# Optimization experiments

Hardware: AMD Instinct MI355X
Metric: run time of the kernel (lower is better)

The kernel has to match this reference:

```python
import jax, jax.numpy as jnp
import numpy as np

HEADS = 4
DIM_HEAD = 64
MAP_SIZE = 16
SCALE = DIM_HEAD ** (-0.5)


def _split_heads(x):
    # torch rearrange 'b (dim_head heads) h w -> b heads (h w) dim_head'
    B, C, H, W = x.shape
    x = x.reshape(B, DIM_HEAD, HEADS, H * W)
    return jnp.transpose(x, (0, 2, 3, 1))  # [B, heads, N, dim_head]


def _merge_heads(x, H, W):
    # torch rearrange 'b heads (h w) dim_head -> b (dim_head heads) h w'
    B, h, N, d = x.shape
    return jnp.transpose(x, (0, 3, 1, 2)).reshape(B, d * h, H, W)


def setup_inputs() -> dict:
    key = jax.random.key(0)
    ks = jax.random.split(key, 6)
    feat = jax.random.normal(ks[0], (4, 256, 96, 96), jnp.float32)
    semantic_map = jax.random.normal(ks[1], (4, 256, 16, 16), jnp.float32)
    # 1x1 conv weights, shape [out_ch, in_ch]; scaled like fan-in init
    W_feat_qv = 0.05 * jax.random.normal(ks[2], (512, 256), jnp.float32)
    W_map_qv = 0.05 * jax.random.normal(ks[3], (512, 256), jnp.float32)
    W_feat_out = 0.05 * jax.random.normal(ks[4], (256, 256), jnp.float32)
    W_map_out = 0.05 * jax.random.normal(ks[5], (256, 256), jnp.float32)
    return {
        "feat": feat,
        "semantic_map": semantic_map,
        "W_feat_qv": W_feat_qv,
        "W_map_qv": W_map_qv,
        "W_feat_out": W_feat_out,
        "W_map_out": W_map_out,
    }


def reference(feat, semantic_map, W_feat_qv, W_map_qv, W_feat_out, W_map_out):
    B, C, H, W = feat.shape
    # 1x1 convs == per-pixel channel matmuls
    fqv = jnp.einsum("oc,bchw->bohw", W_feat_qv, feat)
    feat_q, feat_v = jnp.split(fqv, 2, axis=1)
    mqv = jnp.einsum("oc,bchw->bohw", W_map_qv, semantic_map)
    map_q, map_v = jnp.split(mqv, 2, axis=1)

    feat_q, feat_v = _split_heads(feat_q), _split_heads(feat_v)  # [B,h,N,d]
    map_q, map_v = _split_heads(map_q), _split_heads(map_v)      # [B,h,M,d]

    attn = jnp.einsum("bhid,bhjd->bhij", feat_q, map_q) * SCALE  # [B,h,N,M]
    feat_map_attn = jax.nn.softmax(attn, axis=-1)  # normalize over map tokens j
    map_feat_attn = jax.nn.softmax(attn, axis=-2)  # normalize over feat tokens i

    feat_o = jnp.einsum("bhij,bhjd->bhid", feat_map_attn, map_v)   # [B,h,N,d]
    map_o = jnp.einsum("bhji,bhjd->bhid", map_feat_attn, feat_v)   # [B,h,M,d]

    feat_o = _merge_heads(feat_o, H, W)
    map_o = _merge_heads(map_o, MAP_SIZE, MAP_SIZE)

    feat_out = jnp.einsum("oc,bchw->bohw", W_feat_out, feat_o)
    map_out = jnp.einsum("oc,bchw->bohw", W_map_out, map_o)
    return feat_out, map_out
```

## Files before the change

kernel.cpp:

```cpp
#include <hip/hip_runtime.h>
#include <stdint.h>

#define DI static __device__ __forceinline__

constexpr int NTOK = 9216;
constexpr float ATT_SCALE = 0.125f;

typedef short bf16x8 __attribute__((ext_vector_type(8)));
typedef float f32x4  __attribute__((ext_vector_type(4)));

DI f32x4 mfma16(bf16x8 a, bf16x8 b, f32x4 c) {
  return __builtin_amdgcn_mfma_f32_16x16x32_bf16(a, b, c, 0, 0, 0);
}

DI float lo2f(uint32_t u) { union { uint32_t i; float f; } v; v.i = u << 16; return v.f; }
DI float hi2f(uint32_t u) { union { uint32_t i; float f; } v; v.i = u & 0xffff0000u; return v.f; }
DI float b2f(uint16_t u) { union { uint32_t i; float f; } v; v.i = ((uint32_t)u) << 16; return v.f; }
DI uint16_t f2b(float f) {
  union { float f; uint32_t i; } v; v.f = f;
  uint32_t r = (v.i + 0x7fffu + ((v.i >> 16) & 1u)) >> 16;
  return (uint16_t)r;
}

template<int DT> DI float ld1(const void* p, size_t off) {
  if constexpr (DT) return b2f(((const uint16_t*)p)[off]);
  else              return ((const float*)p)[off];
}
template<int DT> DI void st1(void* p, size_t off, float v) {
  if constexpr (DT) ((uint16_t*)p)[off] = f2b(v);
  else              ((float*)p)[off] = v;
}
template<int DT> DI void load8(const void* p, size_t off, float* o) {
  if constexpr (DT) {
    const uint4 w = *(const uint4*)((const uint16_t*)p + off);
    o[0] = lo2f(w.x); o[1] = hi2f(w.x); o[2] = lo2f(w.y); o[3] = hi2f(w.y);
    o[4] = lo2f(w.z); o[5] = hi2f(w.z); o[6] = lo2f(w.w); o[7] = hi2f(w.w);
  } else {
    const float4 a = *(const float4*)((const float*)p + off);
    const float4 b = *(const float4*)((const float*)p + off + 4);
    o[0] = a.x; o[1] = a.y; o[2] = a.z; o[3] = a.w;
    o[4] = b.x; o[5] = b.y; o[6] = b.z; o[7] = b.w;
  }
}

__global__ void detect_dtype(const uint32_t* __restrict__ w, int* __restrict__ flag) {
  if (threadIdx.x == 0 && blockIdx.x == 0) {
    int cl = 0;
    for (int i = 0; i < 256; ++i) {
      const float b = b2f((uint16_t)(w[i] & 0xffffu));
      const float ab = fabsf(b);
      if (ab > 1e-4f && ab < 0.5f) cl++;
    }
    flag[0] = (cl >= 128) ? 1 : 0;
  }
}

template<int DT>
__global__ __launch_bounds__(256) void prep_w(
    const void* __restrict__ Wfqv, const void* __restrict__ Wfo,
    uint16_t* __restrict__ WqvP, uint16_t* __restrict__ WfoP,
    const int* __restrict__ flag)
{
  if (flag[0] != DT) return;
  const int r = blockIdx.x, c = threadIdx.x;
  if (r < 512) {
    const int sel = r >> 8, within = r & 255;
    const int h = within >> 6, d = within & 63;
    const int src = sel * 256 + d * 4 + h;
    const int q = (c >> 3) & 3, j = c & 7;
    const int kp = (c & ~31) | (q << 3) | ((j + 2 * q) & 7);
    WqvP[(size_t)r * 256 + c] = f2b(ld1<DT>(Wfqv, (size_t)src * 256 + kp));
  } else {
    const int ro = r - 512;
    WfoP[(size_t)ro * 256 + c] =
        f2b(ld1<DT>(Wfo, (size_t)ro * 256 + (c & 63) * 4 + (c >> 6)));
  }
}

constexpr int PB = 264;

template<int DT>
__global__ __launch_bounds__(256) void gemm0_mfma(
    const uint16_t* __restrict__ WqvP, const void* __restrict__ X,
    uint16_t* __restrict__ FQ, uint16_t* __restrict__ FV,
    const int* __restrict__ flag)
{
  if (flag[0] != DT) return;
  __shared__ __align__(16) uint16_t Bsh[32 * PB];
  const int tid = threadIdx.x;
  const int w = tid >> 6, lane = tid & 63;
  const int l = lane & 15, quad = lane >> 4;
  const int n0 = blockIdx.x * 256;
  const int hh = blockIdx.y;
  const int bb = blockIdx.z;
  const size_t bh = (size_t)bb * 4 + hh;

  f32x4 acc[8][4];
  #pragma unroll
  for (int a = 0; a < 8; ++a)
    #pragma unroll
    for (int b = 0; b < 4; ++b) { acc[a][b].x = 0.f; acc[a][b].y = 0.f; acc[a][b].z = 0.f; acc[a][b].w = 0.f; }

  const int cst = tid >> 3;
  const int nst = (tid & 7) * 32;

  for (int ks = 0; ks < 8; ++ks) {
    {
      const size_t gbase = ((size_t)bb * 256 + ks * 32 + cst) * NTOK + n0 + nst;
      #pragma unroll
      for (int q = 0; q < 4; ++q) {
        if constexpr (DT) {
          *(uint4*)(Bsh + cst * PB + nst + q * 8) =
              *(const uint4*)((const uint16_t*)X + gbase + q * 8);
        } else {
          float xv[8];
          load8<0>(X, gbase + q * 8, xv);
          uint16_t pk[8];
          #pragma unroll
          for (int j = 0; j < 8; ++j) pk[j] = f2b(xv[j]);
          *(uint4*)(Bsh + cst * PB + nst + q * 8) = *(const uint4*)pk;
        }
      }
    }
    __syncthreads();
    bf16x8 af[8];
    #pragma unroll
    for (int mt = 0; mt < 8; ++mt) {
      const int arow = (mt >> 2) * 256 + hh * 64 + (mt & 3) * 16 + l;
      af[mt] = *(const bf16x8*)(WqvP + (size_t)arow * 256 + ks * 32 + quad * 8);
    }
    #pragma unroll
    for (int nt = 0; nt < 4; ++nt) {
      const int nl = w * 64 + nt * 16 + l;
      union { uint16_t h[8]; bf16x8 v; } bu;
      #pragma unroll
      for (int j = 0; j < 8; ++j)
        bu.h[j] = Bsh[(quad * 8 + ((j + 2 * quad) & 7)) * PB + nl];
      #pragma unroll
      for (int mt = 0; mt < 8; ++mt)
        acc[mt][nt] = mfma16(af[mt], bu.v, acc[mt][nt]);
    }
    __syncthreads();
  }
  #pragma unroll
  for (int mt = 0; mt < 8; ++mt)
    #pragma unroll
    for (int nt = 0; nt < 4; ++nt) {
      const int n = n0 + w * 64 + nt * 16 + l;
      if (mt < 4) {
        union { uint16_t h[4]; uint2 u; } pk;
        #pragma unroll
        for (int r = 0; r < 4; ++r) pk.h[r] = f2b(acc[mt][nt][r]);
        *(uint2*)(FQ + (bh * NTOK + n) * 64 + mt * 16 + quad * 4) = pk.u;
      } else {
        #pragma unroll
        for (int r = 0; r < 4; ++r)
          FV[(bh * 64 + (mt - 4) * 16 + quad * 4 + r) * NTOK + n] =
              f2b(acc[mt][nt][r]);
      }
    }
}

template<int DT>
__global__ __launch_bounds__(256) void gemm1_mfma(
    const uint16_t* __restrict__ WfoP, const uint16_t* __restrict__ FO,
    void* __restrict__ out, const int* __restrict__ flag)
{
  if (flag[0] != DT) return;
  const int tid = threadIdx.x;
  const int w = tid >> 6, lane = tid & 63;
  const int l = lane & 15, quad = lane >> 4;
  const int n0 = blockIdx.x * 256;
  const int o0 = blockIdx.y * 64;
  const int bb = blockIdx.z;

  f32x4 acc[4][4];
  #pragma unroll
  for (int a = 0; a < 4; ++a)
    #pragma unroll
    for (int b = 0; b < 4; ++b) { acc[a][b].x = 0.f; acc[a][b].y = 0.f; acc[a][b].z = 0.f; acc[a][b].w = 0.f; }

  for (int ks = 0; ks < 8; ++ks) {
    const int h2 = ks >> 1;
    const int doff = (ks & 1) * 32 + quad * 8;
    bf16x8 af[4];
    #pragma unroll
    for (int mt = 0; mt < 4; ++mt)
      af[mt] = *(const bf16x8*)(WfoP + (size_t)(o0 + mt * 16 + l) * 256 + ks * 32 + quad * 8);
    #pragma unroll
    for (int nt = 0; nt < 4; ++nt) {
      const int n = n0 + w * 64 + nt * 16 + l;
      const bf16x8 bv = *(const bf16x8*)(FO + ((size_t)(bb * 4 + h2) * NTOK + n) * 64 + doff);
      #pragma unroll
      for (int mt = 0; mt < 4; ++mt)
        acc[mt][nt] = mfma16(af[mt], bv, acc[mt][nt]);
    }
  }
  #pragma unroll
  for (int mt = 0; mt < 4; ++mt)
    #pragma unroll
    for (int nt = 0; nt < 4; ++nt) {
      const int n = n0 + w * 64 + nt * 16 + l;
      #pragma unroll
      for (int r = 0; r < 4; ++r)
        st1<DT>(out, ((size_t)bb * 256 + o0 + mt * 16 + quad * 4 + r) * NTOK + n,
                acc[mt][nt][r]);
    }
}

template<int DT>
__global__ __launch_bounds__(256) void map_qv(
    const void* __restrict__ Wqv, const void* __restrict__ smap,
    uint16_t* __restrict__ MQ, uint16_t* __restrict__ MVT,
    const int* __restrict__ flag)
{
  if (flag[0] != DT) return;
  const int o = blockIdx.x, bb = blockIdx.y, m = threadIdx.x;
  float acc = 0.f;
  #pragma unroll 8
  for (int c = 0; c < 256; ++c)
    acc += ld1<DT>(Wqv, (size_t)o * 256 + c) *
           ld1<DT>(smap, (size_t)bb * 65536 + (size_t)c * 256 + m);
  const int oc = o & 255;
  const int h = oc & 3, d = oc >> 2;
  if (o < 256) MQ[(((size_t)bb * 4 + h) * 256 + m) * 64 + d] = f2b(acc);
  else         MVT[(((size_t)bb * 4 + h) * 64 + d) * 256 + m] = f2b(acc);
}

constexpr int PJ = 264;
constexpr int PI = 48;
constexpr int NGRP = 32;

__global__ __launch_bounds__(256, 3) void attn_mfma(
    const uint16_t* __restrict__ FQ, const uint16_t* __restrict__ FV,
    const uint16_t* __restrict__ MQ, const uint16_t* __restrict__ MVT,
    uint16_t* __restrict__ FO, uint16_t* __restrict__ P)
{
  __shared__ __align__(16) uint16_t Esh[32 * PJ];
  __shared__ __align__(16) uint16_t ETsh[256 * PI];
  __shared__ float RS[4][32];
  const int tid = threadIdx.x;
  const int w = tid >> 6;
  const int lane = tid & 63;
  const int l = lane & 15, quad = lane >> 4;
  const int blk = blockIdx.x, bh = blockIdx.y;
  const uint16_t* FQh  = FQ  + (size_t)bh * NTOK * 64;
  const uint16_t* FVh  = FV  + (size_t)bh * 64 * NTOK;
  const uint16_t* MQh  = MQ  + (size_t)bh * 256 * 64;
  const uint16_t* MVTh = MVT + (size_t)bh * 64 * 256;
  uint16_t* FOh = FO + (size_t)bh * NTOK * 64;

  f32x4 numacc[4][4];
  #pragma unroll
  for (int a = 0; a < 4; ++a)
    #pragma unroll
    for (int b = 0; b < 4; ++b) { numacc[a][b].x = 0.f; numacc[a][b].y = 0.f; numacc[a][b].z = 0.f; numacc[a][b].w = 0.f; }
  float csum[4] = {0.f, 0.f, 0.f, 0.f};

  for (int t = 0; t < 9; ++t) {
    const int i0 = (blk * 9 + t) * 32;

    bf16x8 qa[2][2];
    #pragma unroll
    for (int mt = 0; mt < 2; ++mt)
      #pragma unroll
      for (int kb = 0; kb < 2; ++kb)
        qa[mt][kb] = *(const bf16x8*)(FQh + (size_t)(i0 + mt * 16 + l) * 64 + kb * 32 + quad * 8);
    float rsum[2][4] = {{0.f,0.f,0.f,0.f},{0.f,0.f,0.f,0.f}};
    #pragma unroll
    for (int jt = 0; jt < 4; ++jt) {
      const int j0 = w * 64 + jt * 16;
      const bf16x8 kb0 = *(const bf16x8*)(MQh + (size_t)(j0 + l) * 64 + quad * 8);
      const bf16x8 kb1 = *(const bf16x8*)(MQh + (size_t)(j0 + l) * 64 + 32 + quad * 8);
      #pragma unroll
      for (int mt = 0; mt < 2; ++mt) {
        f32x4 acc = {0.f, 0.f, 0.f, 0.f};
        acc = mfma16(qa[mt][0], kb0, acc);
        acc = mfma16(qa[mt][1], kb1, acc);
        union { uint16_t h[4]; uint2 u; } pk;
        #pragma unroll
        for (int r = 0; r < 4; ++r) {
          const float e = __expf(acc[r] * ATT_SCALE);
          rsum[mt][r] += e;
          csum[jt] += e;
          pk.h[r] = f2b(e);
          Esh[(mt * 16 + quad * 4 + r) * PJ + j0 + l] = pk.h[r];
        }
        *(uint2*)(ETsh + (size_t)(j0 + l) * PI + mt * 16 + quad * 4) = pk.u;
      }
    }
    #pragma unroll
    for (int mt = 0; mt < 2; ++mt)
      #pragma unroll
      for (int r = 0; r < 4; ++r) {
        float v = rsum[mt][r];
        v += __shfl_xor(v, 1); v += __shfl_xor(v, 2);
        v += __shfl_xor(v, 4); v += __shfl_xor(v, 8);
        if (l == 0) RS[w][mt * 16 + quad * 4 + r] = v;
      }
    __syncthreads();

    {
      float rinv[2];
      #pragma unroll
      for (int nt = 0; nt < 2; ++nt) {
        const int i_ = nt * 16 + l;
        rinv[nt] = 1.f / (RS[0][i_] + RS[1][i_] + RS[2][i_] + RS[3][i_]);
      }
      f32x4 oacc[2];
      oacc[0].x=0.f;oacc[0].y=0.f;oacc[0].z=0.f;oacc[0].w=0.f;
      oacc[1]=oacc[0];
      #pragma unroll
      for (int ks = 0; ks < 8; ++ks) {
        const bf16x8 av = *(const bf16x8*)(MVTh + (size_t)(w * 16 + l) * 256 + ks * 32 + quad * 8);
        #pragma unroll
        for (int nt = 0; nt < 2; ++nt) {
          const bf16x8 bv = *(const bf16x8*)(Esh + (size_t)(nt * 16 + l) * PJ + ks * 32 + quad * 8);
          oacc[nt] = mfma16(av, bv, oacc[nt]);
        }
      }
      #pragma unroll
      for (int nt = 0; nt < 2; ++nt) {
        union { uint16_t h[4]; uint2 u; } pk;
        #pragma unroll
        for (int r = 0; r < 4; ++r) pk.h[r] = f2b(oacc[nt][r] * rinv[nt]);
        *(uint2*)(FOh + (size_t)(i0 + nt * 16 + l) * 64 + w * 16 + quad * 4) = pk.u;
      }
    }

    #pragma unroll
    for (int mt = 0; mt < 4; ++mt) {
      const bf16x8 av = *(const bf16x8*)(FVh + (size_t)(mt * 16 + l) * NTOK + i0 + quad * 8);
      #pragma unroll
      for (int nt2 = 0; nt2 < 4; ++nt2) {
        const bf16x8 bv = *(const bf16x8*)(ETsh + (size_t)(w * 64 + nt2 * 16 + l) * PI + quad * 8);
        numacc[mt][nt2] = mfma16(av, bv, numacc[mt][nt2]);
      }
    }
    __syncthreads();
  }

  uint16_t* Pb = P + ((size_t)bh * NGRP + blk) * 65 * 256;
  #pragma unroll
  for (int mt = 0; mt < 4; ++mt)
    #pragma unroll
    for (int nt2 = 0; nt2 < 4; ++nt2)
      #pragma unroll
      for (int r = 0; r < 4; ++r)
        Pb[(mt * 16 + quad * 4 + r) * 256 + w * 64 + nt2 * 16 + l] =
            f2b(numacc[mt][nt2][r]);
  #pragma unroll
  for (int jt = 0; jt < 4; ++jt) {
    float v = csum[jt];
    v += __shfl_xor(v, 16); v += __shfl_xor(v, 32);
    if (quad == 0) Pb[64 * 256 + w * 64 + jt * 16 + l] = f2b(v);
  }
}

__global__ __launch_bounds__(256) void reduce_map(
    const uint16_t* __restrict__ P, uint16_t* __restrict__ MO)
{
  const int idx = blockIdx.x * 256 + threadIdx.x;
  const int bh = idx >> 14;
  const int d = (idx >> 8) & 63;
  const int j = idx & 255;
  const size_t base = (size_t)bh * NGRP * 65 * 256;
  float num = 0.f, cs = 0.f;
  #pragma unroll 8
  for (int g = 0; g < NGRP; ++g) {
    num += b2f(P[base + ((size_t)g * 65 + d) * 256 + j]);
    cs  += b2f(P[base + ((size_t)g * 65 + 64) * 256 + j]);
  }
  const float v = num / cs;
  const int b = bh >> 2, h = bh & 3;
  MO[((size_t)b * 256 + (d * 4 + h)) * 256 + j] = f2b(v);
}

template<int DT>
__global__ __launch_bounds__(256) void map_out_k(
    const void* __restrict__ Wmo, const uint16_t* __restrict__ MO,
    void* __restrict__ out, const int* __restrict__ flag)
{
  if (flag[0] != DT) return;
  const int o = blockIdx.x, bb = blockIdx.y, m = threadIdx.x;
  float acc = 0.f;
  #pragma unroll 8
  for (int c = 0; c < 256; ++c)
    acc += ld1<DT>(Wmo, (size_t)o * 256 + c) *
           b2f(MO[((size_t)bb * 256 + c) * 256 + m]);
  const size_t MAP_OFS = (size_t)4 * 256 * NTOK;
  st1<DT>(out, MAP_OFS + ((size_t)bb * 256 + o) * 256 + m, acc);
}

extern "C" void kernel_launch(void* const* d_in, const int* in_sizes, int n_in,
                              void* d_out, int out_size, void* d_ws, size_t ws_size,
                              hipStream_t stream) {
  (void)in_sizes; (void)n_in; (void)out_size; (void)ws_size;
  const void* feat = d_in[0];
  const void* smap = d_in[1];
  const void* Wfqv = d_in[2];
  const void* Wmqv = d_in[3];
  const void* Wfo  = d_in[4];
  const void* Wmo  = d_in[5];
  char* ws = (char*)d_ws;

  const size_t BIG = (size_t)16 * 64 * NTOK * 2;
  const size_t SML = (size_t)16 * 256 * 64 * 2;
  const size_t FQ_OFF  = 0;
  const size_t FV_OFF  = FQ_OFF + BIG;
  const size_t MQ_OFF  = FV_OFF + BIG;
  const size_t MVT_OFF = MQ_OFF + SML;
  const size_t MO_OFF  = MVT_OFF + SML;
  const size_t WQP_OFF = MO_OFF + (size_t)4 * 256 * 256 * 2;
  const size_t WFP_OFF = WQP_OFF + (size_t)512 * 256 * 2;
  const size_t FLAG_OFF = WFP_OFF + (size_t)256 * 256 * 2;

  uint16_t* FQ   = (uint16_t*)(ws + FQ_OFF);
  uint16_t* FV   = (uint16_t*)(ws + FV_OFF);
  uint16_t* MQ   = (uint16_t*)(ws + MQ_OFF);
  uint16_t* MVT  = (uint16_t*)(ws + MVT_OFF);
  uint16_t* MO   = (uint16_t*)(ws + MO_OFF);
  uint16_t* WqvP = (uint16_t*)(ws + WQP_OFF);
  uint16_t* WfoP = (uint16_t*)(ws + WFP_OFF);
  int* FLAG   = (int*)(ws + FLAG_OFF);

  uint16_t* P = (uint16_t*)d_out;

  detect_dtype<<<dim3(1), dim3(64), 0, stream>>>((const uint32_t*)Wfqv, FLAG);

  prep_w<0><<<dim3(768), 256, 0, stream>>>(Wfqv, Wfo, WqvP, WfoP, FLAG);
  prep_w<1><<<dim3(768), 256, 0, stream>>>(Wfqv, Wfo, WqvP, WfoP, FLAG);
  gemm0_mfma<0><<<dim3(36, 4, 4), 256, 0, stream>>>(WqvP, feat, FQ, FV, FLAG);
  gemm0_mfma<1><<<dim3(36, 4, 4), 256, 0, stream>>>(WqvP, feat, FQ, FV, FLAG);
  map_qv<0><<<dim3(512, 4), 256, 0, stream>>>(Wmqv, smap, MQ, MVT, FLAG);
  map_qv<1><<<dim3(512, 4), 256, 0, stream>>>(Wmqv, smap, MQ, MVT, FLAG);
  attn_mfma<<<dim3(NGRP, 16), 256, 0, stream>>>(FQ, FV, MQ, MVT, FQ, P);
  reduce_map<<<dim3(1024), 256, 0, stream>>>(P, MO);
  gemm1_mfma<0><<<dim3(36, 4, 4), 256, 0, stream>>>(WfoP, FQ, d_out, FLAG);
  gemm1_mfma<1><<<dim3(36, 4, 4), 256, 0, stream>>>(WfoP, FQ, d_out, FLAG);
  map_out_k<0><<<dim3(256, 4), 256, 0, stream>>>(Wmo, MO, d_out, FLAG);
  map_out_k<1><<<dim3(256, 4), 256, 0, stream>>>(Wmo, MO, d_out, FLAG);
}
```

Baseline: 337.8 us.

## Merge dtype-templated launches, tile FV layout, stage FO via LDS, rebalance attn grid

Replaces the paired per-dtype kernel launches with single kernels that branch on the runtime flag, halving the number of launches. FV is now written in 32-token tiles so the attention kernel reads it contiguously, and FO output goes through an LDS staging buffer so global stores are coalesced 16-byte writes. The attention grid changes from 32 groups of 9 tiles to 36 groups of 8 tiles to fill more CUs, and dtype detection is parallelised across a wavefront. The costs are extra LDS in the attention kernel, which may reduce occupancy, and more partial sums for reduce_map to combine.

```diff
diff --git a/kernel.cpp b/kernel.cpp
--- a/kernel.cpp
+++ b/kernel.cpp
@@ -44,24 +44,23 @@
 }
 
 __global__ void detect_dtype(const uint32_t* __restrict__ w, int* __restrict__ flag) {
-  if (threadIdx.x == 0 && blockIdx.x == 0) {
-    int cl = 0;
-    for (int i = 0; i < 256; ++i) {
-      const float b = b2f((uint16_t)(w[i] & 0xffffu));
-      const float ab = fabsf(b);
-      if (ab > 1e-4f && ab < 0.5f) cl++;
-    }
-    flag[0] = (cl >= 128) ? 1 : 0;
-  }
+  const int l = threadIdx.x;
+  int cl = 0;
+  #pragma unroll
+  for (int i = 0; i < 4; ++i) {
+    const float b = b2f((uint16_t)(w[l + i * 64] & 0xffffu));
+    const float ab = fabsf(b);
+    cl += (ab > 1e-4f && ab < 0.5f) ? 1 : 0;
+  }
+  cl += __shfl_xor(cl, 1);  cl += __shfl_xor(cl, 2);  cl += __shfl_xor(cl, 4);
+  cl += __shfl_xor(cl, 8);  cl += __shfl_xor(cl, 16); cl += __shfl_xor(cl, 32);
+  if (l == 0) flag[0] = (cl >= 128) ? 1 : 0;
 }
 
 template<int DT>
-__global__ __launch_bounds__(256) void prep_w(
-    const void* __restrict__ Wfqv, const void* __restrict__ Wfo,
-    uint16_t* __restrict__ WqvP, uint16_t* __restrict__ WfoP,
-    const int* __restrict__ flag)
-{
-  if (flag[0] != DT) return;
+DI void prep_w_body(const void* __restrict__ Wfqv, const void* __restrict__ Wfo,
+                    uint16_t* __restrict__ WqvP, uint16_t* __restrict__ WfoP)
+{
   const int r = blockIdx.x, c = threadIdx.x;
   if (r < 512) {
     const int sel = r >> 8, within = r & 255;
@@ -76,17 +75,21 @@
         f2b(ld1<DT>(Wfo, (size_t)ro * 256 + (c & 63) * 4 + (c >> 6)));
   }
 }
+__global__ __launch_bounds__(256) void prep_w(
+    const void* Wfqv, const void* Wfo, uint16_t* WqvP, uint16_t* WfoP,
+    const int* __restrict__ flag)
+{
+  if (flag[0]) prep_w_body<1>(Wfqv, Wfo, WqvP, WfoP);
+  else         prep_w_body<0>(Wfqv, Wfo, WqvP, WfoP);
+}
 
 constexpr int PB = 264;
 
 template<int DT>
-__global__ __launch_bounds__(256) void gemm0_mfma(
-    const uint16_t* __restrict__ WqvP, const void* __restrict__ X,
-    uint16_t* __restrict__ FQ, uint16_t* __restrict__ FV,
-    const int* __restrict__ flag)
-{
-  if (flag[0] != DT) return;
-  __shared__ __align__(16) uint16_t Bsh[32 * PB];
+DI void gemm0_body(uint16_t* Bsh, const uint16_t* __restrict__ WqvP,
+                   const void* __restrict__ X,
+                   uint16_t* __restrict__ FQ, uint16_t* __restrict__ FVt)
+{
   const int tid = threadIdx.x;
   const int w = tid >> 6, lane = tid & 63;
   const int l = lane & 15, quad = lane >> 4;
@@ -153,20 +156,27 @@
         for (int r = 0; r < 4; ++r) pk.h[r] = f2b(acc[mt][nt][r]);
         *(uint2*)(FQ + (bh * NTOK + n) * 64 + mt * 16 + quad * 4) = pk.u;
       } else {
+        const int itile = n >> 5, io = n & 31;
         #pragma unroll
         for (int r = 0; r < 4; ++r)
-          FV[(bh * 64 + (mt - 4) * 16 + quad * 4 + r) * NTOK + n] =
+          FVt[(((size_t)bh * 288 + itile) * 64 + (mt - 4) * 16 + quad * 4 + r) * 32 + io] =
               f2b(acc[mt][nt][r]);
       }
     }
 }
+__global__ __launch_bounds__(256) void gemm0_mfma(
+    const uint16_t* WqvP, const void* X, uint16_t* FQ, uint16_t* FVt,
+    const int* __restrict__ flag)
+{
+  __shared__ __align__(16) uint16_t Bsh[32 * PB];
+  if (flag[0]) gemm0_body<1>(Bsh, WqvP, X, FQ, FVt);
+  else         gemm0_body<0>(Bsh, WqvP, X, FQ, FVt);
+}
 
 template<int DT>
-__global__ __launch_bounds__(256) void gemm1_mfma(
-    const uint16_t* __restrict__ WfoP, const uint16_t* __restrict__ FO,
-    void* __restrict__ out, const int* __restrict__ flag)
-{
-  if (flag[0] != DT) return;
+DI void gemm1_body(const uint16_t* __restrict__ WfoP, const uint16_t* __restrict__ FO,
+                   void* __restrict__ out)
+{
   const int tid = threadIdx.x;
   const int w = tid >> 6, lane = tid & 63;
   const int l = lane & 15, quad = lane >> 4;
@@ -207,14 +217,18 @@
                 acc[mt][nt][r]);
     }
 }
+__global__ __launch_bounds__(256) void gemm1_mfma(
+    const uint16_t* WfoP, const uint16_t* FO, void* out,
+    const int* __restrict__ flag)
+{
+  if (flag[0]) gemm1_body<1>(WfoP, FO, out);
+  else         gemm1_body<0>(WfoP, FO, out);
+}
 
 template<int DT>
-__global__ __launch_bounds__(256) void map_qv(
-    const void* __restrict__ Wqv, const void* __restrict__ smap,
-    uint16_t* __restrict__ MQ, uint16_t* __restrict__ MVT,
-    const int* __restrict__ flag)
-{
-  if (flag[0] != DT) return;
+DI void map_qv_body(const void* __restrict__ Wqv, const void* __restrict__ smap,
+                    uint16_t* __restrict__ MQ, uint16_t* __restrict__ MVT)
+{
   const int o = blockIdx.x, bb = blockIdx.y, m = threadIdx.x;
   float acc = 0.f;
   #pragma unroll 8
@@ -226,18 +240,27 @@
   if (o < 256) MQ[(((size_t)bb * 4 + h) * 256 + m) * 64 + d] = f2b(acc);
   else         MVT[(((size_t)bb * 4 + h) * 64 + d) * 256 + m] = f2b(acc);
 }
+__global__ __launch_bounds__(256) void map_qv(
+    const void* Wqv, const void* smap, uint16_t* MQ, uint16_t* MVT,
+    const int* __restrict__ flag)
+{
+  if (flag[0]) map_qv_body<1>(Wqv, smap, MQ, MVT);
+  else         map_qv_body<0>(Wqv, smap, MQ, MVT);
+}
 
 constexpr int PJ = 264;
 constexpr int PI = 48;
-constexpr int NGRP = 32;
+constexpr int PO = 72;
+constexpr int NGRP = 36;
 
 __global__ __launch_bounds__(256, 3) void attn_mfma(
-    const uint16_t* __restrict__ FQ, const uint16_t* __restrict__ FV,
+    const uint16_t* __restrict__ FQ, const uint16_t* __restrict__ FVt,
     const uint16_t* __restrict__ MQ, const uint16_t* __restrict__ MVT,
     uint16_t* __restrict__ FO, uint16_t* __restrict__ P)
 {
   __shared__ __align__(16) uint16_t Esh[32 * PJ];
   __shared__ __align__(16) uint16_t ETsh[256 * PI];
+  __shared__ __align__(16) uint16_t Osh[32 * PO];
   __shared__ float RS[4][32];
   const int tid = threadIdx.x;
   const int w = tid >> 6;
@@ -245,7 +268,7 @@
   const int l = lane & 15, quad = lane >> 4;
   const int blk = blockIdx.x, bh = blockIdx.y;
   const uint16_t* FQh  = FQ  + (size_t)bh * NTOK * 64;
-  const uint16_t* FVh  = FV  + (size_t)bh * 64 * NTOK;
+  const uint16_t* FVth = FVt + (size_t)bh * 288 * 64 * 32;
   const uint16_t* MQh  = MQ  + (size_t)bh * 256 * 64;
   const uint16_t* MVTh = MVT + (size_t)bh * 64 * 256;
   uint16_t* FOh = FO + (size_t)bh * NTOK * 64;
@@ -257,8 +280,9 @@
     for (int b = 0; b < 4; ++b) { numacc[a][b].x = 0.f; numacc[a][b].y = 0.f; numacc[a][b].z = 0.f; numacc[a][b].w = 0.f; }
   float csum[4] = {0.f, 0.f, 0.f, 0.f};
 
-  for (int t = 0; t < 9; ++t) {
-    const int i0 = (blk * 9 + t) * 32;
+  for (int t = 0; t < 8; ++t) {
+    const int it = blk * 8 + t;
+    const int i0 = it * 32;
 
     bf16x8 qa[2][2];
     #pragma unroll
@@ -324,13 +348,13 @@
         union { uint16_t h[4]; uint2 u; } pk;
         #pragma unroll
         for (int r = 0; r < 4; ++r) pk.h[r] = f2b(oacc[nt][r] * rinv[nt]);
-        *(uint2*)(FOh + (size_t)(i0 + nt * 16 + l) * 64 + w * 16 + quad * 4) = pk.u;
+        *(uint2*)(Osh + (nt * 16 + l) * PO + w * 16 + quad * 4) = pk.u;
       }
     }
 
     #pragma unroll
     for (int mt = 0; mt < 4; ++mt) {
-      const bf16x8 av = *(const bf16x8*)(FVh + (size_t)(mt * 16 + l) * NTOK + i0 + quad * 8);
+      const bf16x8 av = *(const bf16x8*)(FVth + ((size_t)it * 64 + mt * 16 + l) * 32 + quad * 8);
       #pragma unroll
       for (int nt2 = 0; nt2 < 4; ++nt2) {
         const bf16x8 bv = *(const bf16x8*)(ETsh + (size_t)(w * 64 + nt2 * 16 + l) * PI + quad * 8);
@@ -338,6 +362,12 @@
       }
     }
     __syncthreads();
+
+    {
+      const int ti = tid >> 3, c = tid & 7;
+      *(uint4*)(FOh + (size_t)(i0 + ti) * 64 + c * 8) =
+          *(const uint4*)(Osh + ti * PO + c * 8);
+    }
   }
 
   uint16_t* Pb = P + ((size_t)bh * NGRP + blk) * 65 * 256;
@@ -366,7 +396,7 @@
   const int j = idx & 255;
   const size_t base = (size_t)bh * NGRP * 65 * 256;
   float num = 0.f, cs = 0.f;
-  #pragma unroll 8
+  #pragma unroll 6
   for (int g = 0; g < NGRP; ++g) {
     num += b2f(P[base + ((size_t)g * 65 + d) * 256 + j]);
     cs  += b2f(P[base + ((size_t)g * 65 + 64) * 256 + j]);
@@ -377,11 +407,9 @@
 }
 
 template<int DT>
-__global__ __launch_bounds__(256) void map_out_k(
-    const void* __restrict__ Wmo, const uint16_t* __restrict__ MO,
-    void* __restrict__ out, const int* __restrict__ flag)
-{
-  if (flag[0] != DT) return;
+DI void map_out_body(const void* __restrict__ Wmo, const uint16_t* __restrict__ MO,
+                     void* __restrict__ out)
+{
   const int o = blockIdx.x, bb = blockIdx.y, m = threadIdx.x;
   float acc = 0.f;
   #pragma unroll 8
@@ -390,6 +418,12 @@
            b2f(MO[((size_t)bb * 256 + c) * 256 + m]);
   const size_t MAP_OFS = (size_t)4 * 256 * NTOK;
   st1<DT>(out, MAP_OFS + ((size_t)bb * 256 + o) * 256 + m, acc);
+}
+__global__ __launch_bounds__(256) void map_out_k(
+    const void* Wmo, const uint16_t* MO, void* out, const int* __restrict__ flag)
+{
+  if (flag[0]) map_out_body<1>(Wmo, MO, out);
+  else         map_out_body<0>(Wmo, MO, out);
 }
 
 extern "C" void kernel_launch(void* const* d_in, const int* in_sizes, int n_in,
@@ -407,8 +441,8 @@
   const size_t BIG = (size_t)16 * 64 * NTOK * 2;
   const size_t SML = (size_t)16 * 256 * 64 * 2;
   const size_t FQ_OFF  = 0;
-  const size_t FV_OFF  = FQ_OFF + BIG;
-  const size_t MQ_OFF  = FV_OFF + BIG;
+  const size_t FVT_OFF = FQ_OFF + BIG;
+  const size_t MQ_OFF  = FVT_OFF + BIG;
   const size_t MVT_OFF = MQ_OFF + SML;
   const size_t MO_OFF  = MVT_OFF + SML;
   const size_t WQP_OFF = MO_OFF + (size_t)4 * 256 * 256 * 2;
@@ -416,7 +450,7 @@
   const size_t FLAG_OFF = WFP_OFF + (size_t)256 * 256 * 2;
 
   uint16_t* FQ   = (uint16_t*)(ws + FQ_OFF);
-  uint16_t* FV   = (uint16_t*)(ws + FV_OFF);
+  uint16_t* FVt  = (uint16_t*)(ws + FVT_OFF);
   uint16_t* MQ   = (uint16_t*)(ws + MQ_OFF);
   uint16_t* MVT  = (uint16_t*)(ws + MVT_OFF);
   uint16_t* MO   = (uint16_t*)(ws + MO_OFF);
@@ -427,17 +461,11 @@
   uint16_t* P = (uint16_t*)d_out;
 
   detect_dtype<<<dim3(1), dim3(64), 0, stream>>>((const uint32_t*)Wfqv, FLAG);
-
-  prep_w<0><<<dim3(768), 256, 0, stream>>>(Wfqv, Wfo, WqvP, WfoP, FLAG);
-  prep_w<1><<<dim3(768), 256, 0, stream>>>(Wfqv, Wfo, WqvP, WfoP, FLAG);
-  gemm0_mfma<0><<<dim3(36, 4, 4), 256, 0, stream>>>(WqvP, feat, FQ, FV, FLAG);
-  gemm0_mfma<1><<<dim3(36, 4, 4), 256, 0, stream>>>(WqvP, feat, FQ, FV, FLAG);
-  map_qv<0><<<dim3(512, 4), 256, 0, stream>>>(Wmqv, smap, MQ, MVT, FLAG);
-  map_qv<1><<<dim3(512, 4), 256, 0, stream>>>(Wmqv, smap, MQ, MVT, FLAG);
-  attn_mfma<<<dim3(NGRP, 16), 256, 0, stream>>>(FQ, FV, MQ, MVT, FQ, P);
+  prep_w<<<dim3(768), 256, 0, stream>>>(Wfqv, Wfo, WqvP, WfoP, FLAG);
+  gemm0_mfma<<<dim3(36, 4, 4), 256, 0, stream>>>(WqvP, feat, FQ, FVt, FLAG);
+  map_qv<<<dim3(512, 4), 256, 0, stream>>>(Wmqv, smap, MQ, MVT, FLAG);
+  attn_mfma<<<dim3(NGRP, 16), 256, 0, stream>>>(FQ, FVt, MQ, MVT, FQ, P);
   reduce_map<<<dim3(1024), 256, 0, stream>>>(P, MO);
-  gemm1_mfma<0><<<dim3(36, 4, 4), 256, 0, stream>>>(WfoP, FQ, d_out, FLAG);
-  gemm1_mfma<1><<<dim3(36, 4, 4), 256, 0, stream>>>(WfoP, FQ, d_out, FLAG);
-  map_out_k<0><<<dim3(256, 4), 256, 0, stream>>>(Wmo, MO, d_out, FLAG);
-  map_out_k<1><<<dim3(256, 4), 256, 0, stream>>>(Wmo, MO, d_out, FLAG);
-}
+  gemm1_mfma<<<dim3(36, 4, 4), 256, 0, stream>>>(WfoP, FQ, d_out, FLAG);
+  map_out_k<<<dim3(256, 4), 256, 0, stream>>>(Wmo, MO, d_out, FLAG);
+}
```

Measured after the change: 314.5 us. 1.07x faster.
